# Kernel optimization log

Measured on AMD Instinct MI355X. Metric: run time of the kernel, lower is better.

The kernel has to match this reference:

```python
import jax, jax.numpy as jnp
import numpy as np
from jax import lax

N_TAPS = 27  # 3x3x3 kernel

def _gather_one(xb, ti, hi, wi):
    # xb: (C,T,H,W); ti/hi/wi: (T,H,W) int32. Zero-fill outside bounds.
    C, T, H, W = xb.shape
    valid = (ti >= 0) & (ti < T) & (hi >= 0) & (hi < H) & (wi >= 0) & (wi < W)
    lin = (jnp.clip(ti, 0, T - 1) * H + jnp.clip(hi, 0, H - 1)) * W + jnp.clip(wi, 0, W - 1)
    v = jnp.take(xb.reshape(C, -1), lin.reshape(-1), axis=1).reshape(C, T, H, W)
    return v * valid.astype(xb.dtype)

_gather = jax.vmap(_gather_one)  # over batch

def _trilinear(x, t, h, w):
    # x: (B,C,T,H,W); t/h/w: (B,T,H,W) float sample coordinates.
    t0, h0, w0 = jnp.floor(t), jnp.floor(h), jnp.floor(w)
    lt, lh, lw = t - t0, h - h0, w - w0
    t0i, h0i, w0i = t0.astype(jnp.int32), h0.astype(jnp.int32), w0.astype(jnp.int32)
    acc = 0.0
    for ti, wt in ((t0i, 1.0 - lt), (t0i + 1, lt)):
        for hi, wh in ((h0i, 1.0 - lh), (h0i + 1, lh)):
            for wi, ww in ((w0i, 1.0 - lw), (w0i + 1, lw)):
                acc = acc + _gather(x, ti, hi, wi) * (wt * wh * ww)[:, None]
    return acc  # (B,C,T,H,W)

def _deform_conv3d(x, offset_w, offset_b, weight):
    # x: (B,Cin,T,H,W). Offset layout: (B, 3, 27, T, H, W), axis1=(dt,dh,dw),
    # tap index k = kt*9 + kh*3 + kw. stride=1, padding=1, dilation=1, no bias.
    off = lax.conv_general_dilated(
        x, offset_w, (1, 1, 1), [(1, 1)] * 3,
        dimension_numbers=("NCDHW", "OIDHW", "NCDHW"))
    off = off + offset_b[None, :, None, None, None]
    B, _, T, H, W = off.shape
    off = off.reshape(B, 3, N_TAPS, T, H, W)
    tg = jnp.arange(T, dtype=x.dtype)[:, None, None]
    hg = jnp.arange(H, dtype=x.dtype)[None, :, None]
    wg = jnp.arange(W, dtype=x.dtype)[None, None, :]
    out = jnp.zeros((B, weight.shape[0], T, H, W), x.dtype)
    for k in range(N_TAPS):
        kt, kh, kw = k // 9, (k // 3) % 3, k % 3
        t = tg + (kt - 1) + off[:, 0, k]
        h = hg + (kh - 1) + off[:, 1, k]
        w = wg + (kw - 1) + off[:, 2, k]
        s = _trilinear(x, t, h, w)  # (B,Cin,T,H,W)
        out = out + jnp.einsum('bcthw,oc->bothw', s, weight[:, :, kt, kh, kw])
    return out

def setup_inputs() -> dict:
    key = jax.random.key(0)
    ks = jax.random.split(key, 4)
    B, T, C, H, W = 1, 4, 64, 128, 128
    x = jax.random.normal(ks[0], (B, T, C, H, W), jnp.float32)
    # small init scale keeps predicted offsets in a realistic +-2px range
    offset_w = jax.random.normal(ks[1], (3 * N_TAPS, C, 3, 3, 3), jnp.float32) * 0.02
    offset_b = jnp.zeros((3 * N_TAPS,), jnp.float32)
    weight = jax.random.normal(ks[2], (C, C, 3, 3, 3), jnp.float32) * 0.02
    gamma = jax.random.normal(ks[3], (1,), jnp.float32) * 0.1
    return {"x": x, "offset_w": offset_w, "offset_b": offset_b,
            "weight": weight, "gamma": gamma}

def reference(x, offset_w, offset_b, weight, gamma):
    xp = jnp.transpose(x, (0, 2, 1, 3, 4))  # (B,C,T,H,W)
    xc = _deform_conv3d(xp, offset_w, offset_b, weight)
    return gamma[0] * jnp.transpose(xc, (0, 2, 1, 3, 4)) + x
```

## Files before the change

kernel.cpp:

```cpp
#include <hip/hip_runtime.h>
#include <cmath>

#define Cc 64
#define Hh 128
#define Ww 128
#define HW_ 16384
#define THW_ 65536
#define CHW_ 1048576
#define NT 27

typedef unsigned short ushort_t;
typedef _Float16 f16x2 __attribute__((ext_vector_type(2)));
typedef _Float16 f16x8 __attribute__((ext_vector_type(8)));
typedef __fp16 fp16x2_alt __attribute__((ext_vector_type(2)));
typedef float floatx4 __attribute__((ext_vector_type(4)));
typedef unsigned uint4v __attribute__((ext_vector_type(4)));

union U32H2 { unsigned u; f16x2 h; };

static __device__ inline ushort_t f2h(float f) {
  union { _Float16 h; ushort_t u; } v;
  v.h = (_Float16)f;
  return v.u;
}

static __device__ inline unsigned pk2(float a) {
  union { fp16x2_alt h; unsigned u; } v;
  v.h = __builtin_amdgcn_cvt_pkrtz(a, a);
  return v.u;
}

static __device__ inline unsigned packh2(float a, float b) {
  return (unsigned)f2h(a) | ((unsigned)f2h(b) << 16);
}

static __device__ inline unsigned rep16(unsigned p) {
#if defined(__has_builtin)
#if __has_builtin(__builtin_amdgcn_perm)
  return __builtin_amdgcn_perm(p, p, 0x01000100u);
#else
  return (p & 0xFFFFu) * 0x10001u;
#endif
#else
  return (p & 0xFFFFu) * 0x10001u;
#endif
}

#if defined(__has_builtin)
#if __has_builtin(__builtin_amdgcn_make_buffer_rsrc) && __has_builtin(__builtin_amdgcn_raw_buffer_load_b32) && __has_builtin(__builtin_amdgcn_raw_buffer_load_b128)
#define USE_BUF 1
#endif
#endif
#ifndef USE_BUF
#define USE_BUF 0
#endif

struct XtBuf {
#if USE_BUF
  __amdgpu_buffer_rsrc_t r;
#else
  const char* p;
#endif
};

static __device__ inline XtBuf mkbuf(const ushort_t* xt) {
  XtBuf b;
#if USE_BUF
  b.r = __builtin_amdgcn_make_buffer_rsrc((void*)xt, (short)0, 8388608, 0x00020000);
#else
  b.p = (const char*)xt;
#endif
  return b;
}

static __device__ inline uint4v xload4(const XtBuf& b, unsigned voff) {
#if USE_BUF
  return __builtin_amdgcn_raw_buffer_load_b128(b.r, (int)voff, 0, 0);
#else
  return *(const uint4v*)(b.p + voff);
#endif
}


__global__ __launch_bounds__(256) void prep_transpose(
    const float* __restrict__ x, ushort_t* __restrict__ xt,
    const float* __restrict__ offset_w,
    const float* __restrict__ weight,
    ushort_t* __restrict__ w2frag,
    ushort_t* __restrict__ wfrag)
{
  __shared__ __align__(16) char smem[33280];
  int tid = threadIdx.x;
  int b = blockIdx.x;
  if (b < 512) {
    float* tile = (float*)smem;
    int t = b >> 7, h = b & 127;
    const float* xrow = x + (size_t)t * CHW_ + (size_t)h * Ww;
    int c0 = tid >> 5;
    int w4 = (tid & 31) * 4;
    #pragma unroll
    for (int p = 0; p < 8; ++p) {
      int c = p * 8 + c0;
      float4 v = *(const float4*)(xrow + (size_t)c * HW_ + w4);
      tile[(w4 + 0) * 65 + c] = v.x;
      tile[(w4 + 1) * 65 + c] = v.y;
      tile[(w4 + 2) * 65 + c] = v.z;
      tile[(w4 + 3) * 65 + c] = v.w;
    }
    __syncthreads();
    int oct = tid & 7;
    int pbase = tid >> 3;
    ushort_t* xrowo = xt + (size_t)(t * HW_ + h * Ww) * 64;
    #pragma unroll
    for (int p = 0; p < 4; ++p) {
      int pos = p * 32 + pbase;
      const float* src = &tile[pos * 65 + oct * 8];
      uint4 u;
      u.x = packh2(src[0], src[1]);
      u.y = packh2(src[2], src[3]);
      u.z = packh2(src[4], src[5]);
      u.w = packh2(src[6], src[7]);
      *(uint4*)(xrowo + (size_t)pos * 64 + oct * 8) = u;
    }
  } else if (b < 523) {
    ushort_t* ldsw = (ushort_t*)smem;
    int i = b - 512;
    const float* src = offset_w + (size_t)i * 13824;
    int limit = 139968 - i * 13824;
    for (int idx = tid * 4; idx < 13824; idx += 1024) {
      float4 v = make_float4(0.f, 0.f, 0.f, 0.f);
      if (idx < limit) v = *(const float4*)(src + idx);
      ldsw[idx + 0] = f2h(v.x);
      ldsw[idx + 1] = f2h(v.y);
      ldsw[idx + 2] = f2h(v.z);
      ldsw[idx + 3] = f2h(v.w);
    }
    __syncthreads();
    int ot = i >> 1;
    int lnlo = (i & 1) * 8;
    for (int ch = tid; ch < 1728; ch += 256) {
      int lnsub = ch & 7;
      int lnhi = (ch >> 3) & 3;
      int kh2 = (ch >> 5) & 1;
      int k = ch >> 6;
      int ln = lnhi * 16 + lnlo + lnsub;
      uint4 u;
      unsigned uu[4];
      #pragma unroll
      for (int q = 0; q < 4; ++q) {
        int c0 = kh2 * 32 + lnhi * 8 + 2 * q;
        ushort_t a = ldsw[lnsub * 1728 + c0 * 27 + k];
        ushort_t bb = ldsw[lnsub * 1728 + (c0 + 1) * 27 + k];
        uu[q] = (unsigned)a | ((unsigned)bb << 16);
      }
      u.x = uu[0]; u.y = uu[1]; u.z = uu[2]; u.w = uu[3];
      *(uint4*)(w2frag + (size_t)(((k * 6 + ot) * 2 + kh2) * 512 + ln * 8)) = u;
    }
  } else {
    ushort_t* ldsw = (ushort_t*)smem;
    int i = b - 523;
    const float* src = weight + (size_t)i * 13824;
    for (int idx = tid * 4; idx < 13824; idx += 1024) {
      float4 v = *(const float4*)(src + idx);
      ldsw[idx + 0] = f2h(v.x);
      ldsw[idx + 1] = f2h(v.y);
      ldsw[idx + 2] = f2h(v.z);
      ldsw[idx + 3] = f2h(v.w);
    }
    __syncthreads();
    int ot = i >> 1;
    int lnlo = (i & 1) * 8;
    for (int ch = tid; ch < 1728; ch += 256) {
      int lnsub = ch & 7;
      int lnhi = (ch >> 3) & 3;
      int kh2 = (ch >> 5) & 1;
      int k = ch >> 6;
      int ln = lnhi * 16 + lnlo + lnsub;
      uint4 u;
      unsigned uu[4];
      #pragma unroll
      for (int q = 0; q < 4; ++q) {
        int c0 = kh2 * 32 + lnhi * 8 + 2 * q;
        ushort_t a = ldsw[lnsub * 1728 + c0 * 27 + k];
        ushort_t bb = ldsw[lnsub * 1728 + (c0 + 1) * 27 + k];
        uu[q] = (unsigned)a | ((unsigned)bb << 16);
      }
      u.x = uu[0]; u.y = uu[1]; u.z = uu[2]; u.w = uu[3];
      *(uint4*)(wfrag + (size_t)(((k * 4 + ot) * 2 + kh2) * 512 + ln * 8)) = u;
    }
  }
}

#define SITE(W, D, A0, A1, A2, A3) \
  { U32H2 wu; wu.u = (W); U32H2 q0, q1, q2, q3; \
    q0.u = (D)[0]; q1.u = (D)[1]; q2.u = (D)[2]; q3.u = (D)[3]; \
    A0 += wu.h * q0.h; A1 += wu.h * q1.h; A2 += wu.h * q2.h; A3 += wu.h * q3.h; }

__global__ __launch_bounds__(256, 3) void fused(
    const float* __restrict__ x,
    const ushort_t* __restrict__ xt,
    const ushort_t* __restrict__ w2frag,
    const float* __restrict__ ob,
    const ushort_t* __restrict__ wfrag,
    const float* __restrict__ gamma,
    float* __restrict__ out)
{
  __shared__ __align__(16) char lds[50768];
  ushort_t* S = (ushort_t*)lds;
  unsigned* pm0 = (unsigned*)(lds + 9216);
  unsigned* pm1 = (unsigned*)(lds + 11264);
  ushort_t* W2lds = (ushort_t*)(lds + 9216);
  ushort_t* Wl0 = (ushort_t*)(lds + 13312);
  ushort_t* Wl1 = (ushort_t*)(lds + 21504);
  float* Obuf = (float*)(lds + 29696);
  float* Dbuf = (float*)lds;
  int tid = threadIdx.x;
  int lane = tid & 63;
  int wavei = __builtin_amdgcn_readfirstlane(tid >> 6);
  int quad = lane >> 4;
  int m16 = lane & 15;
  int g8 = lane >> 3;
  unsigned coff = (unsigned)((lane & 7) * 16);
  int bid0 = blockIdx.x;
  int p0 = ((bid0 & 7) * 128 + (bid0 >> 3)) * 64;
  int t = p0 >> 14;
  int h = (p0 >> 7) & 127;
  int w0 = p0 & 127;
  XtBuf xb = mkbuf(xt);

  {
    floatx4 acc[6];
    #pragma unroll
    for (int i = 0; i < 6; ++i) acc[i] = (floatx4){0.f, 0.f, 0.f, 0.f};

    uint4v pd[2];
    uint4v w2reg[3];

    auto issue = [&](int k) {
      int kt = k / 9, kh = (k / 3) % 3, kw = k % 3;
      int ts = t + kt - 1, hs = h + kh - 1;
      int tsc = min(max(ts, 0), 3);
      int hsc = min(max(hs, 0), 127);
      int sbase = tsc * HW_ + hsc * Ww;
      #pragma unroll
      for (int b = 0; b < 2; ++b) {
        int prow = wavei * 16 + b * 8 + g8;
        int wc = w0 + prow + kw - 1;
        int wcc = min(max(wc, 0), 127);
        pd[b] = xload4(xb, ((unsigned)(sbase + wcc) << 7) + coff);
      }
    };
    auto wload = [&](int k) {
      const uint4v* src = (const uint4v*)(w2frag + (size_t)k * 6144);
      #pragma unroll
      for (int c = 0; c < 3; ++c) w2reg[c] = src[tid + c * 256];
    };
    auto wstore = [&]() {
      uint4v* dst = (uint4v*)W2lds;
      #pragma unroll
      for (int c = 0; c < 3; ++c) dst[tid + c * 256] = w2reg[c];
    };

    wload(0);
    wstore();
    __syncthreads();
    issue(0);

    #pragma unroll 1
    for (int k = 0; k < NT; ++k) {
      bool more = (k + 1 < NT);
      if (more) wload(k + 1);
      __builtin_amdgcn_sched_barrier(0);
      f16x8 wva[6], wvb[6];
      #pragma unroll
      for (int ot = 0; ot < 6; ++ot) {
        wva[ot] = *(const f16x8*)(W2lds + ot * 1024 + lane * 8);
        wvb[ot] = *(const f16x8*)(W2lds + ot * 1024 + 512 + lane * 8);
      }
      int kt = k / 9, kh = (k / 3) % 3, kw = k % 3;
      int ts = t + kt - 1, hs = h + kh - 1;
      bool rowok = ((unsigned)ts < 4u) && ((unsigned)hs < 128u);
      #pragma unroll
      for (int b = 0; b < 2; ++b) {
        int prow = wavei * 16 + b * 8 + g8;
        int wc = w0 + prow + kw - 1;
        bool ok = rowok && ((unsigned)wc < 128u);
        uint4v v = pd[b];
        if (!ok) v = (uint4v){0u, 0u, 0u, 0u};
        *(uint4v*)((char*)S + prow * 144 + coff) = v;
      }
      __builtin_amdgcn_sched_barrier(0);
      const ushort_t* srow = S + (wavei * 16 + m16) * 72 + quad * 8;
      f16x8 af0 = *(const f16x8*)srow;
      f16x8 af1 = *(const f16x8*)(srow + 32);
      #pragma unroll
      for (int ot = 0; ot < 6; ++ot) {
        acc[ot] = __builtin_amdgcn_mfma_f32_16x16x32_f16(af0, wva[ot], acc[ot], 0, 0, 0);
        acc[ot] = __builtin_amdgcn_mfma_f32_16x16x32_f16(af1, wvb[ot], acc[ot], 0, 0, 0);
      }
      __syncthreads();
      if (more) wstore();
      __syncthreads();
      if (more) issue(k + 1);
    }
    #pragma unroll
    for (int ot = 0; ot < 6; ++ot) {
      int oc = ot * 16 + m16;
      if (oc < 81) {
        float bv = ob[oc];
        #pragma unroll
        for (int r = 0; r < 4; ++r)
          Obuf[oc * 65 + wavei * 16 + quad * 4 + r] = acc[ot][r] + bv;
      }
    }
  }

  floatx4 acc[4];
  #pragma unroll
  for (int i = 0; i < 4; ++i) acc[i] = (floatx4){0.f, 0.f, 0.f, 0.f};

  int pl = wavei * 16 + m16;
  int aq = quad >> 1, bq = quad & 1;
  int rowA = wavei * 16 + g8;
  int rowB = rowA + 8;

  uint4v stage[16];
  uint4v wreg[2];

  auto meta = [&](int kk, float dtv, float dhv, float dwv) {
    unsigned* pm = (kk & 1) ? pm1 : pm0;
    int kt = kk / 9, kh = (kk / 3) % 3, kw = kk % 3;
    float tf = (float)(t + kt - 1) + dtv;
    float hf = (float)(h + kh - 1) + dhv;
    float wf = (float)(w0 + pl + kw - 1) + dwv;
    float tF = floorf(tf), hF = floorf(hf), wF = floorf(wf);
    float lt = tf - tF, lh_ = hf - hF, lw_ = wf - wF;
    int t0 = (int)tF, h0 = (int)hF, wq_ = (int)wF;
    int ti = t0 + aq;
    float wt_ = (aq ? lt : 1.f - lt) * (((unsigned)ti < 4u) ? 1.f : 0.f);
    int tic = min(max(ti, 0), 3);
    int hi = h0 + bq;
    float wh_ = (bq ? lh_ : 1.f - lh_) * (((unsigned)hi < 128u) ? 1.f : 0.f);
    int hic = min(max(hi, 0), 127);
    int base2 = tic * HW_ + hic * Ww;
    float bw = wt_ * wh_;
    int wi0 = wq_;
    float ww0 = (1.f - lw_) * (((unsigned)wi0 < 128u) ? 1.f : 0.f);
    int wi0c = min(max(wi0, 0), 127);
    int wi1 = wq_ + 1;
    float ww1 = lw_ * (((unsigned)wi1 < 128u) ? 1.f : 0.f);
    int wi1c = min(max(wi1, 0), 127);
    uint2 mp_;
    mp_.x = ((unsigned)(base2 + wi0c) << 16) | (pk2(bw * ww0) & 0xFFFFu);
    mp_.y = ((unsigned)(base2 + wi1c) << 16) | (pk2(bw * ww1) & 0xFFFFu);
    *(uint2*)&pm[pl * 8 + quad * 2] = mp_;
  };

  auto vof = [&](unsigned p) -> unsigned {
    return ((p >> 9) & 0xFFFFFF80u) + coff;
  };

  auto wload2 = [&](int k) {
    const uint4v* src = (const uint4v*)(wfrag + (size_t)k * 4096);
    wreg[0] = src[tid];
    wreg[1] = src[tid + 256];
  };
  auto wstore2 = [&](int k) {
    uint4v* dst = (uint4v*)((k & 1) ? Wl1 : Wl0);
    dst[tid] = wreg[0];
    dst[tid + 256] = wreg[1];
  };

  auto issueAll = [&](int kk) {
    const unsigned* pmn = (kk & 1) ? pm1 : pm0;
    const uint4* spA = (const uint4*)&pmn[rowA * 8];
    uint4 a0 = spA[0], a1 = spA[1];
    const uint4* spB = (const uint4*)&pmn[rowB * 8];
    uint4 b0 = spB[0], b1 = spB[1];
    stage[0]  = xload4(xb, vof(a0.x));
    stage[1]  = xload4(xb, vof(a0.y));
    stage[2]  = xload4(xb, vof(a0.z));
    stage[3]  = xload4(xb, vof(a0.w));
    stage[4]  = xload4(xb, vof(a1.x));
    stage[5]  = xload4(xb, vof(a1.y));
    stage[6]  = xload4(xb, vof(a1.z));
    stage[7]  = xload4(xb, vof(a1.w));
    stage[8]  = xload4(xb, vof(b0.x));
    stage[9]  = xload4(xb, vof(b0.y));
    stage[10] = xload4(xb, vof(b0.z));
    stage[11] = xload4(xb, vof(b0.w));
    stage[12] = xload4(xb, vof(b1.x));
    stage[13] = xload4(xb, vof(b1.y));
    stage[14] = xload4(xb, vof(b1.z));
    stage[15] = xload4(xb, vof(b1.w));
  };

  auto consumeA = [&](int kk) {
    const unsigned* pmc = (kk & 1) ? pm1 : pm0;
    const uint4* wp = (const uint4*)&pmc[rowA * 8];
    uint4 w03 = wp[0], w47 = wp[1];
    U32H2 z; z.u = 0;
    f16x2 e0 = z.h, e1 = z.h, e2 = z.h, e3 = z.h;
    f16x2 o0 = z.h, o1 = z.h, o2 = z.h, o3 = z.h;
    SITE(rep16(w03.x), stage[0], e0, e1, e2, e3)
    SITE(rep16(w03.y), stage[1], o0, o1, o2, o3)
    SITE(rep16(w03.z), stage[2], e0, e1, e2, e3)
    SITE(rep16(w03.w), stage[3], o0, o1, o2, o3)
    SITE(rep16(w47.x), stage[4], e0, e1, e2, e3)
    SITE(rep16(w47.y), stage[5], o0, o1, o2, o3)
    SITE(rep16(w47.z), stage[6], e0, e1, e2, e3)
    SITE(rep16(w47.w), stage[7], o0, o1, o2, o3)
    U32H2 r0, r1, r2, r3;
    r0.h = e0 + o0; r1.h = e1 + o1; r2.h = e2 + o2; r3.h = e3 + o3;
    uint4v res = {r0.u, r1.u, r2.u, r3.u};
    *(uint4v*)((char*)S + rowA * 144 + coff) = res;
  };
  auto consumeB = [&](int kk) {
    const unsigned* pmc = (kk & 1) ? pm1 : pm0;
    const uint4* wp = (const uint4*)&pmc[rowB * 8];
    uint4 w03 = wp[0], w47 = wp[1];
    U32H2 z; z.u = 0;
    f16x2 e0 = z.h, e1 = z.h, e2 = z.h, e3 = z.h;
    f16x2 o0 = z.h, o1 = z.h, o2 = z.h, o3 = z.h;
    SITE(rep16(w03.x), stage[8],  e0, e1, e2, e3)
    SITE(rep16(w03.y), stage[9],  o0, o1, o2, o3)
    SITE(rep16(w03.z), stage[10], e0, e1, e2, e3)
    SITE(rep16(w03.w), stage[11], o0, o1, o2, o3)
    SITE(rep16(w47.x), stage[12], e0, e1, e2, e3)
    SITE(rep16(w47.y), stage[13], o0, o1, o2, o3)
    SITE(rep16(w47.z), stage[14], e0, e1, e2, e3)
    SITE(rep16(w47.w), stage[15], o0, o1, o2, o3)
    U32H2 r0, r1, r2, r3;
    r0.h = e0 + o0; r1.h = e1 + o1; r2.h = e2 + o2; r3.h = e3 + o3;
    uint4v res = {r0.u, r1.u, r2.u, r3.u};
    *(uint4v*)((char*)S + rowB * 144 + coff) = res;
  };

  __syncthreads();
  wload2(0);
  {
    float dt0 = Obuf[(0 * NT + 0) * 65 + pl];
    float dh0 = Obuf[(1 * NT + 0) * 65 + pl];
    float dw0 = Obuf[(2 * NT + 0) * 65 + pl];
    meta(0, dt0, dh0, dw0);
  }
  wstore2(0);
  __syncthreads();
  issueAll(0);

  #pragma unroll 1
  for (int k = 0; k < NT; ++k) {
    bool more = (k + 1 < NT);
    if (more) wload2(k + 1);
    if (more) {
      float dt_n = Obuf[(0 * NT + (k + 1)) * 65 + pl];
      float dh_n = Obuf[(1 * NT + (k + 1)) * 65 + pl];
      float dw_n = Obuf[(2 * NT + (k + 1)) * 65 + pl];
      meta(k + 1, dt_n, dh_n, dw_n);
    }
    __builtin_amdgcn_sched_barrier(0);
    consumeA(k);
    consumeB(k);
    __builtin_amdgcn_sched_barrier(0);
    f16x8 wva[4], wvb[4];
    {
      const ushort_t* Wl = (k & 1) ? Wl1 : Wl0;
      #pragma unroll
      for (int ot = 0; ot < 4; ++ot) {
        wva[ot] = *(const f16x8*)(Wl + ot * 1024 + lane * 8);
        wvb[ot] = *(const f16x8*)(Wl + ot * 1024 + 512 + lane * 8);
      }
    }
    if (more) wstore2(k + 1);
    const ushort_t* srow = S + (wavei * 16 + m16) * 72 + quad * 8;
    f16x8 af0 = *(const f16x8*)srow;
    f16x8 af1 = *(const f16x8*)(srow + 32);
    #pragma unroll
    for (int ot = 0; ot < 4; ++ot) {
      acc[ot] = __builtin_amdgcn_mfma_f32_16x16x32_f16(af0, wva[ot], acc[ot], 0, 0, 0);
      acc[ot] = __builtin_amdgcn_mfma_f32_16x16x32_f16(af1, wvb[ot], acc[ot], 0, 0, 0);
    }
    __syncthreads();
    if (more) issueAll(k + 1);
  }
  __syncthreads();
  #pragma unroll
  for (int ot = 0; ot < 4; ++ot)
    #pragma unroll
    for (int r = 0; r < 4; ++r)
      Dbuf[(ot * 16 + m16) * 65 + wavei * 16 + quad * 4 + r] = acc[ot][r];
  __syncthreads();
  float g = gamma[0];
  for (int i = threadIdx.x; i < 64 * 64; i += 256) {
    int oc = i >> 6, p = i & 63;
    size_t oi = (size_t)t * CHW_ + (size_t)oc * HW_ + (size_t)h * Ww + w0 + p;
    out[oi] = fmaf(g, Dbuf[oc * 65 + p], x[oi]);
  }
}

extern "C" void kernel_launch(void* const* d_in, const int* in_sizes, int n_in,
                              void* d_out, int out_size, void* d_ws, size_t ws_size,
                              hipStream_t stream) {
  (void)in_sizes; (void)n_in; (void)out_size; (void)ws_size;
  const float* x        = (const float*)d_in[0];
  const float* offset_w = (const float*)d_in[1];
  const float* offset_b = (const float*)d_in[2];
  const float* weight   = (const float*)d_in[3];
  const float* gamma    = (const float*)d_in[4];
  float* out = (float*)d_out;
  float* wsf = (float*)d_ws;
  ushort_t* xt     = (ushort_t*)(wsf + 5308416);
  ushort_t* wfrag  = (ushort_t*)(wsf + 7405568);
  ushort_t* w2frag = (ushort_t*)(wsf + 7460864);

  hipLaunchKernelGGL(prep_transpose, dim3(531), dim3(256), 0, stream,
                     x, xt, offset_w, weight, w2frag, wfrag);
  hipLaunchKernelGGL(fused, dim3(1024), dim3(256), 0, stream,
                     x, xt, w2frag, offset_b, wfrag, gamma, out);
}
```

Baseline: 204.4 us.

## Load gathered samples directly in MFMA A-fragment layout, removing LDS staging

Each lane now gathers the channels for its own MFMA row (pixel pl, channel group by quad) and feeds the blended values straight into the MFMA A operands. This removes the S staging buffer and its LDS write and read per tap in both the offset-conv and the deformable phase. Each lane's loads now cover two 64-byte halves of one site instead of one 16-byte chunk per row, which changes the coalescing pattern. LDS use per block also shrinks, which could allow more blocks per CU.

Result: slower. 320.1 us (+56.6%).

```diff
diff --git a/kernel.cpp b/kernel.cpp
--- a/kernel.cpp
+++ b/kernel.cpp
@@ -17,6 +17,7 @@
 typedef unsigned uint4v __attribute__((ext_vector_type(4)));
 
 union U32H2 { unsigned u; f16x2 h; };
+union U4F8 { uint4v u; f16x8 h; };
 
 static __device__ inline ushort_t f2h(float f) {
   union { _Float16 h; ushort_t u; } v;
@@ -205,22 +206,20 @@
     const float* __restrict__ gamma,
     float* __restrict__ out)
 {
-  __shared__ __align__(16) char lds[50768];
-  ushort_t* S = (ushort_t*)lds;
-  unsigned* pm0 = (unsigned*)(lds + 9216);
-  unsigned* pm1 = (unsigned*)(lds + 11264);
-  ushort_t* W2lds = (ushort_t*)(lds + 9216);
-  ushort_t* Wl0 = (ushort_t*)(lds + 13312);
-  ushort_t* Wl1 = (ushort_t*)(lds + 21504);
-  float* Obuf = (float*)(lds + 29696);
+  __shared__ __align__(16) char lds[41540];
+  unsigned* pm0 = (unsigned*)lds;
+  unsigned* pm1 = (unsigned*)(lds + 2048);
+  ushort_t* Wl0 = (ushort_t*)(lds + 4096);
+  ushort_t* Wl1 = (ushort_t*)(lds + 12288);
+  ushort_t* W2lds = (ushort_t*)lds;
+  float* Obuf = (float*)(lds + 20480);
   float* Dbuf = (float*)lds;
   int tid = threadIdx.x;
   int lane = tid & 63;
   int wavei = __builtin_amdgcn_readfirstlane(tid >> 6);
   int quad = lane >> 4;
   int m16 = lane & 15;
-  int g8 = lane >> 3;
-  unsigned coff = (unsigned)((lane & 7) * 16);
+  unsigned cbase = (unsigned)quad * 16u;
   int bid0 = blockIdx.x;
   int p0 = ((bid0 & 7) * 128 + (bid0 >> 3)) * 64;
   int t = p0 >> 14;
@@ -228,6 +227,8 @@
   int w0 = p0 & 127;
   XtBuf xb = mkbuf(xt);
 
+  int pl = wavei * 16 + m16;
+
   {
     floatx4 acc[6];
     #pragma unroll
@@ -241,14 +242,11 @@
       int ts = t + kt - 1, hs = h + kh - 1;
       int tsc = min(max(ts, 0), 3);
       int hsc = min(max(hs, 0), 127);
-      int sbase = tsc * HW_ + hsc * Ww;
-      #pragma unroll
-      for (int b = 0; b < 2; ++b) {
-        int prow = wavei * 16 + b * 8 + g8;
-        int wc = w0 + prow + kw - 1;
-        int wcc = min(max(wc, 0), 127);
-        pd[b] = xload4(xb, ((unsigned)(sbase + wcc) << 7) + coff);
-      }
+      int wc = w0 + pl + kw - 1;
+      int wcc = min(max(wc, 0), 127);
+      unsigned ro = ((unsigned)(tsc * HW_ + hsc * Ww + wcc) << 7) + cbase;
+      pd[0] = xload4(xb, ro);
+      pd[1] = xload4(xb, ro + 64u);
     };
     auto wload = [&](int k) {
       const uint4v* src = (const uint4v*)(w2frag + (size_t)k * 6144);
@@ -279,24 +277,17 @@
       }
       int kt = k / 9, kh = (k / 3) % 3, kw = k % 3;
       int ts = t + kt - 1, hs = h + kh - 1;
-      bool rowok = ((unsigned)ts < 4u) && ((unsigned)hs < 128u);
-      #pragma unroll
-      for (int b = 0; b < 2; ++b) {
-        int prow = wavei * 16 + b * 8 + g8;
-        int wc = w0 + prow + kw - 1;
-        bool ok = rowok && ((unsigned)wc < 128u);
-        uint4v v = pd[b];
-        if (!ok) v = (uint4v){0u, 0u, 0u, 0u};
-        *(uint4v*)((char*)S + prow * 144 + coff) = v;
-      }
+      int wc = w0 + pl + kw - 1;
+      bool ok = ((unsigned)ts < 4u) && ((unsigned)hs < 128u) && ((unsigned)wc < 128u);
+      uint4v zz = (uint4v){0u, 0u, 0u, 0u};
+      U4F8 a0, a1;
+      a0.u = ok ? pd[0] : zz;
+      a1.u = ok ? pd[1] : zz;
       __builtin_amdgcn_sched_barrier(0);
-      const ushort_t* srow = S + (wavei * 16 + m16) * 72 + quad * 8;
-      f16x8 af0 = *(const f16x8*)srow;
-      f16x8 af1 = *(const f16x8*)(srow + 32);
       #pragma unroll
       for (int ot = 0; ot < 6; ++ot) {
-        acc[ot] = __builtin_amdgcn_mfma_f32_16x16x32_f16(af0, wva[ot], acc[ot], 0, 0, 0);
-        acc[ot] = __builtin_amdgcn_mfma_f32_16x16x32_f16(af1, wvb[ot], acc[ot], 0, 0, 0);
+        acc[ot] = __builtin_amdgcn_mfma_f32_16x16x32_f16(a0.h, wva[ot], acc[ot], 0, 0, 0);
+        acc[ot] = __builtin_amdgcn_mfma_f32_16x16x32_f16(a1.h, wvb[ot], acc[ot], 0, 0, 0);
       }
       __syncthreads();
       if (more) wstore();
@@ -319,13 +310,11 @@
   #pragma unroll
   for (int i = 0; i < 4; ++i) acc[i] = (floatx4){0.f, 0.f, 0.f, 0.f};
 
-  int pl = wavei * 16 + m16;
   int aq = quad >> 1, bq = quad & 1;
-  int rowA = wavei * 16 + g8;
-  int rowB = rowA + 8;
 
   uint4v stage[16];
   uint4v wreg[2];
+  uint4 mk03, mk47;
 
   auto meta = [&](int kk, float dtv, float dhv, float dwv) {
     unsigned* pm = (kk & 1) ? pm1 : pm0;
@@ -356,8 +345,8 @@
     *(uint2*)&pm[pl * 8 + quad * 2] = mp_;
   };
 
-  auto vof = [&](unsigned p) -> unsigned {
-    return ((p >> 9) & 0xFFFFFF80u) + coff;
+  auto vsite = [&](unsigned p) -> unsigned {
+    return (p >> 9) & 0xFFFFFF80u;
   };
 
   auto wload2 = [&](int k) {
@@ -373,67 +362,17 @@
 
   auto issueAll = [&](int kk) {
     const unsigned* pmn = (kk & 1) ? pm1 : pm0;
-    const uint4* spA = (const uint4*)&pmn[rowA * 8];
-    uint4 a0 = spA[0], a1 = spA[1];
-    const uint4* spB = (const uint4*)&pmn[rowB * 8];
-    uint4 b0 = spB[0], b1 = spB[1];
-    stage[0]  = xload4(xb, vof(a0.x));
-    stage[1]  = xload4(xb, vof(a0.y));
-    stage[2]  = xload4(xb, vof(a0.z));
-    stage[3]  = xload4(xb, vof(a0.w));
-    stage[4]  = xload4(xb, vof(a1.x));
-    stage[5]  = xload4(xb, vof(a1.y));
-    stage[6]  = xload4(xb, vof(a1.z));
-    stage[7]  = xload4(xb, vof(a1.w));
-    stage[8]  = xload4(xb, vof(b0.x));
-    stage[9]  = xload4(xb, vof(b0.y));
-    stage[10] = xload4(xb, vof(b0.z));
-    stage[11] = xload4(xb, vof(b0.w));
-    stage[12] = xload4(xb, vof(b1.x));
-    stage[13] = xload4(xb, vof(b1.y));
-    stage[14] = xload4(xb, vof(b1.z));
-    stage[15] = xload4(xb, vof(b1.w));
-  };
-
-  auto consumeA = [&](int kk) {
-    const unsigned* pmc = (kk & 1) ? pm1 : pm0;
-    const uint4* wp = (const uint4*)&pmc[rowA * 8];
-    uint4 w03 = wp[0], w47 = wp[1];
-    U32H2 z; z.u = 0;
-    f16x2 e0 = z.h, e1 = z.h, e2 = z.h, e3 = z.h;
-    f16x2 o0 = z.h, o1 = z.h, o2 = z.h, o3 = z.h;
-    SITE(rep16(w03.x), stage[0], e0, e1, e2, e3)
-    SITE(rep16(w03.y), stage[1], o0, o1, o2, o3)
-    SITE(rep16(w03.z), stage[2], e0, e1, e2, e3)
-    SITE(rep16(w03.w), stage[3], o0, o1, o2, o3)
-    SITE(rep16(w47.x), stage[4], e0, e1, e2, e3)
-    SITE(rep16(w47.y), stage[5], o0, o1, o2, o3)
-    SITE(rep16(w47.z), stage[6], e0, e1, e2, e3)
-    SITE(rep16(w47.w), stage[7], o0, o1, o2, o3)
-    U32H2 r0, r1, r2, r3;
-    r0.h = e0 + o0; r1.h = e1 + o1; r2.h = e2 + o2; r3.h = e3 + o3;
-    uint4v res = {r0.u, r1.u, r2.u, r3.u};
-    *(uint4v*)((char*)S + rowA * 144 + coff) = res;
-  };
-  auto consumeB = [&](int kk) {
-    const unsigned* pmc = (kk & 1) ? pm1 : pm0;
-    const uint4* wp = (const uint4*)&pmc[rowB * 8];
-    uint4 w03 = wp[0], w47 = wp[1];
-    U32H2 z; z.u = 0;
-    f16x2 e0 = z.h, e1 = z.h, e2 = z.h, e3 = z.h;
-    f16x2 o0 = z.h, o1 = z.h, o2 = z.h, o3 = z.h;
-    SITE(rep16(w03.x), stage[8],  e0, e1, e2, e3)
-    SITE(rep16(w03.y), stage[9],  o0, o1, o2, o3)
-    SITE(rep16(w03.z), stage[10], e0, e1, e2, e3)
-    SITE(rep16(w03.w), stage[11], o0, o1, o2, o3)
-    SITE(rep16(w47.x), stage[12], e0, e1, e2, e3)
-    SITE(rep16(w47.y), stage[13], o0, o1, o2, o3)
-    SITE(rep16(w47.z), stage[14], e0, e1, e2, e3)
-    SITE(rep16(w47.w), stage[15], o0, o1, o2, o3)
-    U32H2 r0, r1, r2, r3;
-    r0.h = e0 + o0; r1.h = e1 + o1; r2.h = e2 + o2; r3.h = e3 + o3;
-    uint4v res = {r0.u, r1.u, r2.u, r3.u};
-    *(uint4v*)((char*)S + rowB * 144 + coff) = res;
+    mk03 = *(const uint4*)&pmn[pl * 8];
+    mk47 = *(const uint4*)&pmn[pl * 8 + 4];
+    unsigned s;
+    s = vsite(mk03.x) + cbase; stage[0]  = xload4(xb, s); stage[1]  = xload4(xb, s + 64u);
+    s = vsite(mk03.y) + cbase; stage[2]  = xload4(xb, s); stage[3]  = xload4(xb, s + 64u);
+    s = vsite(mk03.z) + cbase; stage[4]  = xload4(xb, s); stage[5]  = xload4(xb, s + 64u);
+    s = vsite(mk03.w) + cbase; stage[6]  = xload4(xb, s); stage[7]  = xload4(xb, s + 64u);
+    s = vsite(mk47.x) + cbase; stage[8]  = xload4(xb, s); stage[9]  = xload4(xb, s + 64u);
+    s = vsite(mk47.y) + cbase; stage[10] = xload4(xb, s); stage[11] = xload4(xb, s + 64u);
+    s = vsite(mk47.z) + cbase; stage[12] = xload4(xb, s); stage[13] = xload4(xb, s + 64u);
+    s = vsite(mk47.w) + cbase; stage[14] = xload4(xb, s); stage[15] = xload4(xb, s + 64u);
   };
 
   __syncthreads();
@@ -459,8 +398,39 @@
       meta(k + 1, dt_n, dh_n, dw_n);
     }
     __builtin_amdgcn_sched_barrier(0);
-    consumeA(k);
-    consumeB(k);
+    U4F8 af0, af1;
+    {
+      U32H2 z; z.u = 0;
+      f16x2 e0 = z.h, e1 = z.h, e2 = z.h, e3 = z.h;
+      f16x2 o0 = z.h, o1 = z.h, o2 = z.h, o3 = z.h;
+      SITE(rep16(mk03.x), stage[0],  e0, e1, e2, e3)
+      SITE(rep16(mk03.y), stage[2],  o0, o1, o2, o3)
+      SITE(rep16(mk03.z), stage[4],  e0, e1, e2, e3)
+      SITE(rep16(mk03.w), stage[6],  o0, o1, o2, o3)
+      SITE(rep16(mk47.x), stage[8],  e0, e1, e2, e3)
+      SITE(rep16(mk47.y), stage[10], o0, o1, o2, o3)
+      SITE(rep16(mk47.z), stage[12], e0, e1, e2, e3)
+      SITE(rep16(mk47.w), stage[14], o0, o1, o2, o3)
+      U32H2 r0, r1, r2, r3;
+      r0.h = e0 + o0; r1.h = e1 + o1; r2.h = e2 + o2; r3.h = e3 + o3;
+      af0.u = (uint4v){r0.u, r1.u, r2.u, r3.u};
+    }
+    {
+      U32H2 z; z.u = 0;
+      f16x2 e0 = z.h, e1 = z.h, e2 = z.h, e3 = z.h;
+      f16x2 o0 = z.h, o1 = z.h, o2 = z.h, o3 = z.h;
+      SITE(rep16(mk03.x), stage[1],  e0, e1, e2, e3)
+      SITE(rep16(mk03.y), stage[3],  o0, o1, o2, o3)
+      SITE(rep16(mk03.z), stage[5],  e0, e1, e2, e3)
+      SITE(rep16(mk03.w), stage[7],  o0, o1, o2, o3)
+      SITE(rep16(mk47.x), stage[9],  e0, e1, e2, e3)
+      SITE(rep16(mk47.y), stage[11], o0, o1, o2, o3)
+      SITE(rep16(mk47.z), stage[13], e0, e1, e2, e3)
+      SITE(rep16(mk47.w), stage[15], o0, o1, o2, o3)
+      U32H2 r0, r1, r2, r3;
+      r0.h = e0 + o0; r1.h = e1 + o1; r2.h = e2 + o2; r3.h = e3 + o3;
+      af1.u = (uint4v){r0.u, r1.u, r2.u, r3.u};
+    }
     __builtin_amdgcn_sched_barrier(0);
     f16x8 wva[4], wvb[4];
     {
@@ -472,13 +442,10 @@
       }
     }
     if (more) wstore2(k + 1);
-    const ushort_t* srow = S + (wavei * 16 + m16) * 72 + quad * 8;
-    f16x8 af0 = *(const f16x8*)srow;
-    f16x8 af1 = *(const f16x8*)(srow + 32);
     #pragma unroll
     for (int ot = 0; ot < 4; ++ot) {
-      acc[ot] = __builtin_amdgcn_mfma_f32_16x16x32_f16(af0, wva[ot], acc[ot], 0, 0, 0);
-      acc[ot] = __builtin_amdgcn_mfma_f32_16x16x32_f16(af1, wvb[ot], acc[ot], 0, 0, 0);
+      acc[ot] = __builtin_amdgcn_mfma_f32_16x16x32_f16(af0.h, wva[ot], acc[ot], 0, 0, 0);
+      acc[ot] = __builtin_amdgcn_mfma_f32_16x16x32_f16(af1.h, wvb[ot], acc[ot], 0, 0, 0);
     }
     __syncthreads();
     if (more) issueAll(k + 1);
```
